# Kernel tuning notes

Hardware: AMD Instinct MI355X
Metric: run time of the kernel (lower is better)

Reference implementation:

```python
import jax, jax.numpy as jnp
import numpy as np

D_MODEL = 1024
N_HEADS = 16
HEAD_DIM = D_MODEL // N_HEADS


def setup_inputs() -> dict:
    key = jax.random.key(0)
    ks = jax.random.split(key, 11)
    B, S = 2, 2048
    s = 1.0 / np.sqrt(D_MODEL)
    return {
        "query": jax.random.normal(ks[0], (B, S, D_MODEL), jnp.float32),
        "key": jax.random.normal(ks[1], (B, S, D_MODEL), jnp.float32),
        "value": jax.random.normal(ks[2], (B, S, D_MODEL), jnp.float32),
        "Wq": jax.random.normal(ks[3], (D_MODEL, D_MODEL), jnp.float32) * s,
        "bq": jnp.zeros((D_MODEL,), jnp.float32),
        "Wk": jax.random.normal(ks[4], (D_MODEL, D_MODEL), jnp.float32) * s,
        "bk": jnp.zeros((D_MODEL,), jnp.float32),
        "Wv": jax.random.normal(ks[5], (D_MODEL, D_MODEL), jnp.float32) * s,
        "bv": jnp.zeros((D_MODEL,), jnp.float32),
        "Wo": jax.random.normal(ks[6], (D_MODEL, D_MODEL), jnp.float32) * s,
        "bo": jnp.zeros((D_MODEL,), jnp.float32),
    }


def reference(query, key, value, Wq, bq, Wk, bk, Wv, bv, Wo, bo):
    B, S, _ = query.shape
    H, Dh = N_HEADS, HEAD_DIM
    scale = jnp.sqrt(jnp.asarray(Dh, query.dtype))
    # projections (torch Linear: x @ W.T + b)
    Q = (query @ Wq.T + bq).reshape(B, S, H, Dh).transpose(0, 2, 1, 3)  # [B,H,S,Dh]
    K = (key @ Wk.T + bk).reshape(B, S, H, Dh).transpose(0, 2, 1, 3)
    V = (value @ Wv.T + bv).reshape(B, S, H, Dh).transpose(0, 2, 1, 3)
    # full score matrix, matching the naive formulation
    energy = jnp.einsum("bhqd,bhkd->bhqk", Q, K) / scale  # [B,H,S,S]
    attn = jax.nn.softmax(energy, axis=-1)
    # dropout: eval mode -> identity
    out = jnp.einsum("bhqk,bhkd->bhqd", attn, V)  # [B,H,S,Dh]
    out = out.transpose(0, 2, 1, 3).reshape(B, S, H * Dh)
    return out @ Wo.T + bo
```

## Files before the change

kernel.cpp:

```cpp
#include <hip/hip_runtime.h>
#include <hip/hip_bf16.h>
#include <stdint.h>


typedef unsigned short u16;
typedef __attribute__((ext_vector_type(8))) short bf16x8;
typedef __attribute__((ext_vector_type(4))) float f32x4;

#define MFMA16 __builtin_amdgcn_mfma_f32_16x16x32_bf16

#define GM 4096
#define GN 1024
#define GK 1024
#define S_LEN 2048
#define NH 16
#define DH 64
#define KVBLK 64
#define PSTR 72
#define TILE_ELEMS (128 * 64)

__device__ __forceinline__ u16 f2bf(float f) {
    union { float f; uint32_t u; } v; v.f = f;
    return (u16)((v.u + 0x7fffu + ((v.u >> 16) & 1u)) >> 16);
}

__device__ __forceinline__ u16 f2bf_hw(float f) {
    __hip_bfloat16 h = __float2bfloat16(f);
    return *(u16*)&h;
}

__global__ __launch_bounds__(256) void cvt_bf16_kernel(const float* __restrict__ src,
                                                       u16* __restrict__ dst, int n8,
                                                       float scale) {
    int i = blockIdx.x * 256 + threadIdx.x;
    if (i >= n8) return;
    const f32x4* s = (const f32x4*)src + (size_t)i * 2;
    f32x4 a = s[0], b = s[1];
    union { bf16x8 v; u16 u[8]; } o;
    o.u[0] = f2bf(a[0] * scale); o.u[1] = f2bf(a[1] * scale);
    o.u[2] = f2bf(a[2] * scale); o.u[3] = f2bf(a[3] * scale);
    o.u[4] = f2bf(b[0] * scale); o.u[5] = f2bf(b[1] * scale);
    o.u[6] = f2bf(b[2] * scale); o.u[7] = f2bf(b[3] * scale);
    *(bf16x8*)(dst + (size_t)i * 8) = o.v;
}

__global__ __launch_bounds__(256) void scale_f32_kernel(const float* __restrict__ src,
                                                        float* __restrict__ dst, int n,
                                                        float scale) {
    int i = blockIdx.x * 256 + threadIdx.x;
    if (i < n) dst[i] = src[i] * scale;
}

__device__ __forceinline__ void gemm_core(const u16* __restrict__ A,
                                          const u16* __restrict__ W,
                                          const float* __restrict__ bias,
                                          void* __restrict__ Cout, int mode,
                                          u16* As, u16* Bs) {
    const int t  = threadIdx.x;
    const int l  = t & 63;
    const int w  = t >> 6;
    const int wr = w >> 1, wc = w & 1;
    const int cl = l & 15, g = l >> 4;
    const int rx = cl & 7;
    const int mbase = blockIdx.y * 128;
    const int nbase = blockIdx.x * 128;

    f32x4 acc[4][4];
    f32x4 zero = {0.f, 0.f, 0.f, 0.f};
    #pragma unroll
    for (int i = 0; i < 4; ++i)
        #pragma unroll
        for (int j = 0; j < 4; ++j) acc[i][j] = zero;

    #define GSTAGE(buf, kt)                                                                 \
        do {                                                                                \
            _Pragma("unroll")                                                               \
            for (int r = 0; r < 4; ++r) {                                                   \
                int c = r * 256 + t;                                                        \
                int row = c >> 3;                                                           \
                int c8 = (c & 7) ^ (row & 7);                                               \
                __builtin_amdgcn_global_load_lds(                                           \
                    (const __attribute__((address_space(1))) void*)(A + (size_t)(mbase + row) * GK + (kt) + c8 * 8), \
                    (__attribute__((address_space(3))) void*)(As + (buf) * TILE_ELEMS + c * 8), 16, 0, 0); \
                __builtin_amdgcn_global_load_lds(                                           \
                    (const __attribute__((address_space(1))) void*)(W + (size_t)(nbase + row) * GK + (kt) + c8 * 8), \
                    (__attribute__((address_space(3))) void*)(Bs + (buf) * TILE_ELEMS + c * 8), 16, 0, 0); \
            }                                                                               \
        } while (0)

    GSTAGE(0, 0);
    __syncthreads();

    int cur = 0;
    for (int kt = 0; kt < GK; kt += 64) {
        if (kt + 64 < GK) GSTAGE(cur ^ 1, kt + 64);

        const u16* Asb = As + cur * TILE_ELEMS;
        const u16* Bsb = Bs + cur * TILE_ELEMS;
        #pragma unroll
        for (int ks = 0; ks < 2; ++ks) {
            bf16x8 af[4], bfr[4];
            #pragma unroll
            for (int mi = 0; mi < 4; ++mi) {
                int row = wr * 64 + mi * 16 + cl;
                af[mi] = *(const bf16x8*)&Asb[row * 64 + ((ks * 4 + g) ^ rx) * 8];
            }
            #pragma unroll
            for (int nj = 0; nj < 4; ++nj) {
                int row = wc * 64 + nj * 16 + cl;
                bfr[nj] = *(const bf16x8*)&Bsb[row * 64 + ((ks * 4 + g) ^ rx) * 8];
            }
            #pragma unroll
            for (int mi = 0; mi < 4; ++mi)
                #pragma unroll
                for (int nj = 0; nj < 4; ++nj)
                    acc[mi][nj] = MFMA16(af[mi], bfr[nj], acc[mi][nj], 0, 0, 0);
        }
        __syncthreads();
        cur ^= 1;
    }
    #undef GSTAGE

    #pragma unroll
    for (int mi = 0; mi < 4; ++mi) {
        #pragma unroll
        for (int nj = 0; nj < 4; ++nj) {
            int n = nbase + wc * 64 + nj * 16 + cl;
            float bv = bias[n];
            #pragma unroll
            for (int r = 0; r < 4; ++r) {
                int m = mbase + wr * 64 + mi * 16 + g * 4 + r;
                float vv = acc[mi][nj][r] + bv;
                if (mode == 2) {
                    ((float*)Cout)[(size_t)m * GN + n] = vv;
                } else {
                    int b = m >> 11, s = m & 2047;
                    int h = n >> 6, dh = n & 63;
                    if (mode == 0)
                        ((u16*)Cout)[(((size_t)(b * NH + h)) * S_LEN + s) * DH + dh] = f2bf(vv);
                    else
                        ((u16*)Cout)[(((size_t)(b * NH + h)) * DH + dh) * S_LEN + s] = f2bf(vv);
                }
            }
        }
    }
}

__global__ __launch_bounds__(256) void proj_gemm(
        const u16* __restrict__ qbf, const u16* __restrict__ kbf, const u16* __restrict__ vbf,
        const u16* __restrict__ Wqb, const u16* __restrict__ Wkb, const u16* __restrict__ Wvb,
        const float* __restrict__ bq, const float* __restrict__ bk, const float* __restrict__ bv,
        u16* __restrict__ Qb, u16* __restrict__ Kb, u16* __restrict__ Vtb) {
    __shared__ u16 As[2 * TILE_ELEMS];
    __shared__ u16 Bs[2 * TILE_ELEMS];
    int z = blockIdx.z;
    const u16* A   = (z == 0) ? qbf : (z == 1) ? kbf : vbf;
    const u16* W   = (z == 0) ? Wqb : (z == 1) ? Wkb : Wvb;
    const float* b = (z == 0) ? bq  : (z == 1) ? bk  : bv;
    u16* C         = (z == 0) ? Qb  : (z == 1) ? Kb  : Vtb;
    gemm_core(A, W, b, (void*)C, (z == 2) ? 1 : 0, As, Bs);
}

__global__ __launch_bounds__(256) void out_gemm(const u16* __restrict__ A,
                                                const u16* __restrict__ W,
                                                const float* __restrict__ bias,
                                                float* __restrict__ C) {
    __shared__ u16 As[2 * TILE_ELEMS];
    __shared__ u16 Bs[2 * TILE_ELEMS];
    gemm_core(A, W, bias, (void*)C, 2, As, Bs);
}

__global__ __launch_bounds__(512, 4) void attn_kernel(const u16* __restrict__ Q,
                                                      const u16* __restrict__ Kb,
                                                      const u16* __restrict__ Vt,
                                                      u16* __restrict__ O) {
    __shared__ u16 Ks[2][KVBLK * 64];
    __shared__ u16 Vs[2][KVBLK * 64];
    __shared__ u16 Pl[8][16 * PSTR];

    const int t = threadIdx.x, l = t & 63, w = t >> 6;
    const int cl = l & 15, g = l >> 4;
    const int bh = blockIdx.x;
    const int b = bh >> 4, h = bh & 15;
    const int qw = blockIdx.y * 128 + w * 16;

    const u16* Qp = Q  + ((size_t)bh * S_LEN + qw) * DH;
    const u16* Kp = Kb + (size_t)bh * S_LEN * DH;
    const u16* Vp = Vt + (size_t)bh * DH * S_LEN;

    bf16x8 qf0 = *(const bf16x8*)(Qp + (size_t)cl * DH + g * 8);
    bf16x8 qf1 = *(const bf16x8*)(Qp + (size_t)cl * DH + 32 + g * 8);

    float rs[4] = {0.f, 0.f, 0.f, 0.f};
    f32x4 oacc[4];
    f32x4 zero = {0.f, 0.f, 0.f, 0.f};
    #pragma unroll
    for (int tt = 0; tt < 4; ++tt) oacc[tt] = zero;

    u16* P = Pl[w];

    const int srow = t >> 3;
    const int sc8  = (t & 7) ^ (srow & 7);
    const u16* Kg = Kp + (size_t)srow * DH + sc8 * 8;
    const u16* Vg = Vp + (size_t)srow * S_LEN + sc8 * 8;

    #define STAGE(buf, kvoff)                                                            \
        do {                                                                             \
            __builtin_amdgcn_global_load_lds(                                            \
                (const __attribute__((address_space(1))) void*)(Kg + (size_t)(kvoff) * DH), \
                (__attribute__((address_space(3))) void*)(&Ks[buf][0] + t * 8), 16, 0, 0); \
            __builtin_amdgcn_global_load_lds(                                            \
                (const __attribute__((address_space(1))) void*)(Vg + (kvoff)),           \
                (__attribute__((address_space(3))) void*)(&Vs[buf][0] + t * 8), 16, 0, 0); \
        } while (0)

    STAGE(0, 0);
    __syncthreads();

    const int NT = S_LEN / KVBLK;
    int cur = 0;
    for (int it = 0; it < NT; ++it) {
        if (it + 1 < NT) STAGE(cur ^ 1, (it + 1) * KVBLK);

        const u16* Ksb = &Ks[cur][0];
        const u16* Vsb = &Vs[cur][0];

        f32x4 s[4];
        #pragma unroll
        for (int j = 0; j < 4; ++j) s[j] = zero;
        __builtin_amdgcn_s_setprio(1);
        #pragma unroll
        for (int j = 0; j < 4; ++j) {
            int row = j * 16 + cl, rx = row & 7;
            bf16x8 k0 = *(const bf16x8*)&Ksb[row * 64 + ((g)     ^ rx) * 8];
            bf16x8 k1 = *(const bf16x8*)&Ksb[row * 64 + ((4 + g) ^ rx) * 8];
            s[j] = MFMA16(qf0, k0, s[j], 0, 0, 0);
            s[j] = MFMA16(qf1, k1, s[j], 0, 0, 0);
        }
        __builtin_amdgcn_s_setprio(0);

        #pragma unroll
        for (int j = 0; j < 4; ++j) {
            #pragma unroll
            for (int r = 0; r < 4; ++r) {
                float p = __builtin_amdgcn_exp2f(s[j][r]);
                rs[r] += p;
                P[(g * 4 + r) * PSTR + j * 16 + cl] = f2bf_hw(p);
            }
        }

        bf16x8 pf[2];
        #pragma unroll
        for (int ks = 0; ks < 2; ++ks)
            pf[ks] = *(const bf16x8*)&P[cl * PSTR + ks * 32 + g * 8];

        __builtin_amdgcn_s_setprio(1);
        #pragma unroll
        for (int tt = 0; tt < 4; ++tt) {
            int row = tt * 16 + cl, rx = row & 7;
            #pragma unroll
            for (int ks = 0; ks < 2; ++ks) {
                bf16x8 vf = *(const bf16x8*)&Vsb[row * 64 + ((ks * 4 + g) ^ rx) * 8];
                oacc[tt] = MFMA16(pf[ks], vf, oacc[tt], 0, 0, 0);
            }
        }
        __builtin_amdgcn_s_setprio(0);

        __syncthreads();
        cur ^= 1;
    }
    #undef STAGE

    #pragma unroll
    for (int d = 1; d < 16; d <<= 1)
        #pragma unroll
        for (int r = 0; r < 4; ++r)
            rs[r] += __shfl_xor(rs[r], d, 64);

    #pragma unroll
    for (int tt = 0; tt < 4; ++tt) {
        #pragma unroll
        for (int r = 0; r < 4; ++r) {
            int q = qw + g * 4 + r;
            float val = oacc[tt][r] / rs[r];
            O[((size_t)b * S_LEN + q) * GN + h * DH + tt * 16 + cl] = f2bf(val);
        }
    }
}

extern "C" void kernel_launch(void* const* d_in, const int* in_sizes, int n_in,
                              void* d_out, int out_size, void* d_ws, size_t ws_size,
                              hipStream_t stream) {
    const float* query = (const float*)d_in[0];
    const float* key   = (const float*)d_in[1];
    const float* value = (const float*)d_in[2];
    const float* Wq = (const float*)d_in[3];
    const float* bq = (const float*)d_in[4];
    const float* Wk = (const float*)d_in[5];
    const float* bk = (const float*)d_in[6];
    const float* Wv = (const float*)d_in[7];
    const float* bv = (const float*)d_in[8];
    const float* Wo = (const float*)d_in[9];
    const float* bo = (const float*)d_in[10];
    float* out = (float*)d_out;

    const float QSCALE = 0.125f * 1.4426950408889634f;

    u16* ws = (u16*)d_ws;
    const size_t MD = (size_t)GM * GN;
    const size_t WW = (size_t)GN * GK;
    u16* qbf = ws;
    u16* kbf = qbf + MD;
    u16* vbf = kbf + MD;
    u16* Wqb = vbf + MD;
    u16* Wkb = Wqb + WW;
    u16* Wvb = Wkb + WW;
    u16* Wob = Wvb + WW;
    u16* Qb  = Wob + WW;
    u16* Kbf = Qb  + MD;
    u16* Vtb = Kbf + MD;
    u16* Ob  = Vtb + MD;
    float* bqs = (float*)(Ob + MD);

    cvt_bf16_kernel<<<(int)(MD / 8 / 256), 256, 0, stream>>>(query, qbf, (int)(MD / 8), 1.f);
    cvt_bf16_kernel<<<(int)(MD / 8 / 256), 256, 0, stream>>>(key,   kbf, (int)(MD / 8), 1.f);
    cvt_bf16_kernel<<<(int)(MD / 8 / 256), 256, 0, stream>>>(value, vbf, (int)(MD / 8), 1.f);
    cvt_bf16_kernel<<<(int)(WW / 8 / 256), 256, 0, stream>>>(Wq, Wqb, (int)(WW / 8), QSCALE);
    cvt_bf16_kernel<<<(int)(WW / 8 / 256), 256, 0, stream>>>(Wk, Wkb, (int)(WW / 8), 1.f);
    cvt_bf16_kernel<<<(int)(WW / 8 / 256), 256, 0, stream>>>(Wv, Wvb, (int)(WW / 8), 1.f);
    cvt_bf16_kernel<<<(int)(WW / 8 / 256), 256, 0, stream>>>(Wo, Wob, (int)(WW / 8), 1.f);
    scale_f32_kernel<<<(GN + 255) / 256, 256, 0, stream>>>(bq, bqs, GN, QSCALE);

    dim3 gproj(GN / 128, GM / 128, 3);
    proj_gemm<<<gproj, 256, 0, stream>>>(qbf, kbf, vbf, Wqb, Wkb, Wvb,
                                         bqs, bk, bv, Qb, Kbf, Vtb);

    dim3 gattn(2 * NH, S_LEN / 128);
    attn_kernel<<<gattn, 512, 0, stream>>>(Qb, Kbf, Vtb, Ob);

    dim3 gout(GN / 128, GM / 128);
    out_gemm<<<gout, 256, 0, stream>>>(Ob, Wob, bo, out);
}
```

Measured before the change: 155.8 us.

## Merge conversion launches and triple-buffer K/V tiles in attention

```diff
diff --git a/kernel.cpp b/kernel.cpp
--- a/kernel.cpp
+++ b/kernel.cpp
@@ -29,26 +29,37 @@
     return *(u16*)&h;
 }
 
-__global__ __launch_bounds__(256) void cvt_bf16_kernel(const float* __restrict__ src,
-                                                       u16* __restrict__ dst, int n8,
-                                                       float scale) {
-    int i = blockIdx.x * 256 + threadIdx.x;
-    if (i >= n8) return;
-    const f32x4* s = (const f32x4*)src + (size_t)i * 2;
+__global__ __launch_bounds__(256) void cvt_all_kernel(
+        const float* __restrict__ q, const float* __restrict__ k, const float* __restrict__ v,
+        const float* __restrict__ Wq, const float* __restrict__ Wk,
+        const float* __restrict__ Wv, const float* __restrict__ Wo,
+        const float* __restrict__ bq,
+        u16* __restrict__ qbf, u16* __restrict__ kbf, u16* __restrict__ vbf,
+        u16* __restrict__ Wqb, u16* __restrict__ Wkb, u16* __restrict__ Wvb,
+        u16* __restrict__ Wob, float* __restrict__ bqs, float qscale) {
+    int bid = blockIdx.x;
+    if (bid >= 8192) {
+        int i = (bid - 8192) * 256 + (int)threadIdx.x;
+        if (i < GN) bqs[i] = bq[i] * qscale;
+        return;
+    }
+    const float* src; u16* dst; float scale = 1.f; int off;
+    if      (bid < 2048) { src = q;  dst = qbf; off = bid; }
+    else if (bid < 4096) { src = k;  dst = kbf; off = bid - 2048; }
+    else if (bid < 6144) { src = v;  dst = vbf; off = bid - 4096; }
+    else if (bid < 6656) { src = Wq; dst = Wqb; off = bid - 6144; scale = qscale; }
+    else if (bid < 7168) { src = Wk; dst = Wkb; off = bid - 6656; }
+    else if (bid < 7680) { src = Wv; dst = Wvb; off = bid - 7168; }
+    else                 { src = Wo; dst = Wob; off = bid - 7680; }
+    size_t i = (size_t)off * 256 + threadIdx.x;
+    const f32x4* s = (const f32x4*)src + i * 2;
     f32x4 a = s[0], b = s[1];
-    union { bf16x8 v; u16 u[8]; } o;
+    union { bf16x8 v8; u16 u[8]; } o;
     o.u[0] = f2bf(a[0] * scale); o.u[1] = f2bf(a[1] * scale);
     o.u[2] = f2bf(a[2] * scale); o.u[3] = f2bf(a[3] * scale);
     o.u[4] = f2bf(b[0] * scale); o.u[5] = f2bf(b[1] * scale);
     o.u[6] = f2bf(b[2] * scale); o.u[7] = f2bf(b[3] * scale);
-    *(bf16x8*)(dst + (size_t)i * 8) = o.v;
-}
-
-__global__ __launch_bounds__(256) void scale_f32_kernel(const float* __restrict__ src,
-                                                        float* __restrict__ dst, int n,
-                                                        float scale) {
-    int i = blockIdx.x * 256 + threadIdx.x;
-    if (i < n) dst[i] = src[i] * scale;
+    *(bf16x8*)(dst + i * 8) = o.v8;
 }
 
 __device__ __forceinline__ void gemm_core(const u16* __restrict__ A,
@@ -174,8 +185,8 @@
                                                       const u16* __restrict__ Kb,
                                                       const u16* __restrict__ Vt,
                                                       u16* __restrict__ O) {
-    __shared__ u16 Ks[2][KVBLK * 64];
-    __shared__ u16 Vs[2][KVBLK * 64];
+    __shared__ u16 Ks[3][KVBLK * 64];
+    __shared__ u16 Vs[3][KVBLK * 64];
     __shared__ u16 Pl[8][16 * PSTR];
 
     const int t = threadIdx.x, l = t & 63, w = t >> 6;
@@ -215,12 +226,17 @@
         } while (0)
 
     STAGE(0, 0);
-    __syncthreads();
+    STAGE(1, KVBLK);
+    asm volatile("s_waitcnt vmcnt(2)" ::: "memory");
+    __builtin_amdgcn_s_barrier();
 
     const int NT = S_LEN / KVBLK;
     int cur = 0;
     for (int it = 0; it < NT; ++it) {
-        if (it + 1 < NT) STAGE(cur ^ 1, (it + 1) * KVBLK);
+        if (it + 2 < NT) {
+            int nb = cur + 2; if (nb >= 3) nb -= 3;
+            STAGE(nb, (it + 2) * KVBLK);
+        }
 
         const u16* Ksb = &Ks[cur][0];
         const u16* Vsb = &Vs[cur][0];
@@ -266,8 +282,12 @@
         }
         __builtin_amdgcn_s_setprio(0);
 
-        __syncthreads();
-        cur ^= 1;
+        if (it + 2 < NT) {
+            asm volatile("s_waitcnt vmcnt(2)\n\ts_barrier" ::: "memory");
+        } else {
+            asm volatile("s_waitcnt vmcnt(0)\n\ts_barrier" ::: "memory");
+        }
+        cur = (cur + 1 == 3) ? 0 : cur + 1;
     }
     #undef STAGE
 
@@ -322,14 +342,9 @@
     u16* Ob  = Vtb + MD;
     float* bqs = (float*)(Ob + MD);
 
-    cvt_bf16_kernel<<<(int)(MD / 8 / 256), 256, 0, stream>>>(query, qbf, (int)(MD / 8), 1.f);
-    cvt_bf16_kernel<<<(int)(MD / 8 / 256), 256, 0, stream>>>(key,   kbf, (int)(MD / 8), 1.f);
-    cvt_bf16_kernel<<<(int)(MD / 8 / 256), 256, 0, stream>>>(value, vbf, (int)(MD / 8), 1.f);
-    cvt_bf16_kernel<<<(int)(WW / 8 / 256), 256, 0, stream>>>(Wq, Wqb, (int)(WW / 8), QSCALE);
-    cvt_bf16_kernel<<<(int)(WW / 8 / 256), 256, 0, stream>>>(Wk, Wkb, (int)(WW / 8), 1.f);
-    cvt_bf16_kernel<<<(int)(WW / 8 / 256), 256, 0, stream>>>(Wv, Wvb, (int)(WW / 8), 1.f);
-    cvt_bf16_kernel<<<(int)(WW / 8 / 256), 256, 0, stream>>>(Wo, Wob, (int)(WW / 8), 1.f);
-    scale_f32_kernel<<<(GN + 255) / 256, 256, 0, stream>>>(bq, bqs, GN, QSCALE);
+    cvt_all_kernel<<<8196, 256, 0, stream>>>(query, key, value, Wq, Wk, Wv, Wo, bq,
+                                             qbf, kbf, vbf, Wqb, Wkb, Wvb, Wob,
+                                             bqs, QSCALE);
 
     dim3 gproj(GN / 128, GM / 128, 3);
     proj_gemm<<<gproj, 256, 0, stream>>>(qbf, kbf, vbf, Wqb, Wkb, Wvb,
```

Result: faster. 142.6 us (-8.5%).
